# Kernel optimization log

Hardware: AMD Instinct MI355X
Metric: run time of the kernel (lower is better)

## Reference

```python
import jax, jax.numpy as jnp
import numpy as np

D_MODEL = 1024
NUM_HEADS = 16
D_HEAD = D_MODEL // NUM_HEADS


def _rope(x):
    """Rotary embedding, lucidrains interleaved convention, applied along axis -2.

    x: (..., n, d). Positions are arange(n); freq_i = 10000**(-2i/d), each freq
    repeated twice (interleaved); rotate_half swaps adjacent pairs (-x2, x1).
    """
    n, d = x.shape[-2], x.shape[-1]
    inv_freq = 1.0 / (10000.0 ** (jnp.arange(0, d, 2, dtype=jnp.float32) / d))  # (d/2,)
    freqs = jnp.arange(n, dtype=jnp.float32)[:, None] * inv_freq[None, :]       # (n, d/2)
    emb = jnp.repeat(freqs, 2, axis=-1)                                         # (n, d)
    cos, sin = jnp.cos(emb).astype(x.dtype), jnp.sin(emb).astype(x.dtype)
    xp = x.reshape(x.shape[:-1] + (d // 2, 2))
    rot = jnp.stack([-xp[..., 1], xp[..., 0]], axis=-1).reshape(x.shape)
    return x * cos + rot * sin


def setup_inputs() -> dict:
    key = jax.random.key(0)
    ks = jax.random.split(key, 11)
    B, S = 4, 2048
    mk = lambda k, shape: (jax.random.normal(k, shape, dtype=jnp.float32) * 0.02)
    return {
        "query": jax.random.normal(ks[0], (B, S, D_MODEL), dtype=jnp.float32),
        "key": jax.random.normal(ks[1], (B, S, D_MODEL), dtype=jnp.float32),
        "value": jax.random.normal(ks[2], (B, S, D_MODEL), dtype=jnp.float32),
        "Wq": mk(ks[3], (D_MODEL, D_MODEL)), "bq": jnp.zeros((D_MODEL,), jnp.float32),
        "Wk": mk(ks[4], (D_MODEL, D_MODEL)), "bk": jnp.zeros((D_MODEL,), jnp.float32),
        "Wv": mk(ks[5], (D_MODEL, D_MODEL)), "bv": jnp.zeros((D_MODEL,), jnp.float32),
        "Wo": mk(ks[6], (D_MODEL, D_MODEL)), "bo": jnp.zeros((D_MODEL,), jnp.float32),
    }


def reference(query, key, value, Wq, bq, Wk, bk, Wv, bv, Wo, bo):
    B, S, _ = query.shape
    H, dh = NUM_HEADS, D_HEAD
    # projections (torch Linear: x @ W.T + b)
    q = (query @ Wq.T + bq).reshape(B, S, H, dh)           # (b, t, h, d)
    k = (key @ Wk.T + bk).reshape(B, S, H, dh).transpose(0, 2, 1, 3)   # (b, h, t, d)
    v = (value @ Wv.T + bv).reshape(B, S, H, dh).transpose(0, 2, 1, 3)  # (b, h, t, d)
    # Faithful to source: query rotated along axis -2 = HEADS axis (pre-permute),
    # key rotated along axis -2 = time axis.
    q = _rope(q)                                            # positions over heads (source quirk)
    k = _rope(k)                                            # positions over time
    q = q.transpose(0, 2, 1, 3)                             # (b, h, t, d)
    scores = jnp.einsum("bhqd,bhkd->bhqk", q, k) / jnp.sqrt(jnp.float32(D_MODEL))
    attn = jax.nn.softmax(scores, axis=-1)
    ctx = jnp.einsum("bhqk,bhkd->bhqd", attn, v)            # (b, h, t, d)
    ctx = ctx.transpose(0, 2, 1, 3).reshape(B, S, H * dh)   # (b, t, d_model)
    return ctx @ Wo.T + bo
```

## Files before the change

### kernel.cpp

```cpp
#include <hip/hip_runtime.h>

using u16 = unsigned short;
typedef __bf16 bf16x8 __attribute__((ext_vector_type(8)));
typedef __bf16 bf16x2 __attribute__((ext_vector_type(2)));
typedef float f32x4 __attribute__((ext_vector_type(4)));

#if __has_builtin(__builtin_amdgcn_exp2f)
#define QSCALE 0.04508422468443852f
#define FEXP(x) __builtin_amdgcn_exp2f(x)
#else
#define QSCALE 0.03125f
#define FEXP(x) __expf(x)
#endif

__device__ __forceinline__ u16 f2bf(float f) {
  unsigned u = __builtin_bit_cast(unsigned, f);
  u += 0x7FFFu + ((u >> 16) & 1u);
  return (u16)(u >> 16);
}

#define GLD_LDS16(g, l)                                                                   \
  __builtin_amdgcn_global_load_lds((const __attribute__((address_space(1))) void*)(g),    \
                                   (__attribute__((address_space(3))) void*)(l), 16, 0, 0)

template <int LOG2NB>
__global__ void cvt_multi(const float* __restrict__ i0, const float* __restrict__ i1,
                          const float* __restrict__ i2, const float* __restrict__ i3,
                          u16* __restrict__ o0, u16* __restrict__ o1, u16* __restrict__ o2,
                          u16* __restrict__ o3, int n4) {
  const int which = blockIdx.x >> LOG2NB;
  const float* in = which == 0 ? i0 : which == 1 ? i1 : which == 2 ? i2 : i3;
  u16* out = which == 0 ? o0 : which == 1 ? o1 : which == 2 ? o2 : o3;
  int i = (blockIdx.x & ((1 << LOG2NB) - 1)) * blockDim.x + threadIdx.x;
  const int st = (1 << LOG2NB) * blockDim.x;
  for (; i < n4; i += st) {
    float4 v = reinterpret_cast<const float4*>(in)[i];
    ushort4 o = make_ushort4(f2bf(v.x), f2bf(v.y), f2bf(v.z), f2bf(v.w));
    reinterpret_cast<ushort4*>(out)[i] = o;
  }
}

template <int EPI>
__global__ __launch_bounds__(512, 4) void gemm_bt(const u16* __restrict__ A,
                                                  const u16* __restrict__ Bt,
                                                  const float* __restrict__ bias,
                                                  void* __restrict__ outp) {
  __shared__ u16 lA[3][128 * 32];
  __shared__ u16 lB[3][128 * 32];
  const int tid = threadIdx.x;
  const int l = tid & 63, w = tid >> 6;
  const int wr = w >> 2, wc = w & 3;
  const int l15 = l & 15, lg = l >> 4;
  const int rsw = (l15 >> 1) & 3;
  const int bid = ((blockIdx.x & 7) << 6) | (blockIdx.x >> 3);
  const int br = bid >> 3, bc = bid & 7;

  f32x4 acc[4][2];
#pragma unroll
  for (int m = 0; m < 4; ++m)
#pragma unroll
    for (int n = 0; n < 2; ++n) acc[m][n] = f32x4{0.f, 0.f, 0.f, 0.f};

  const int srow = tid >> 2;
  const int gch = (tid & 3) ^ ((tid >> 3) & 3);
  const u16* Abase = A + (size_t)(br * 128 + srow) * 1024 + gch * 8;
  const u16* Bbase = Bt + (size_t)(bc * 128 + srow) * 1024 + gch * 8;

  auto stage = [&](int buf, int kk) {
    GLD_LDS16(Abase + kk, &lA[buf][tid * 8]);
    GLD_LDS16(Bbase + kk, &lB[buf][tid * 8]);
  };

  auto compute = [&](int cur) {
    const int c = ((lg ^ rsw) << 3);
    bf16x8 af[4], bfr[2];
#pragma unroll
    for (int m = 0; m < 4; ++m)
      af[m] = *reinterpret_cast<const bf16x8*>(&lA[cur][(wr * 64 + m * 16 + l15) * 32 + c]);
#pragma unroll
    for (int n = 0; n < 2; ++n)
      bfr[n] = *reinterpret_cast<const bf16x8*>(&lB[cur][(wc * 32 + n * 16 + l15) * 32 + c]);
#pragma unroll
    for (int m = 0; m < 4; ++m)
#pragma unroll
      for (int n = 0; n < 2; ++n)
        acc[m][n] = __builtin_amdgcn_mfma_f32_16x16x32_bf16(af[m], bfr[n], acc[m][n], 0, 0, 0);
  };

  stage(0, 0);
  stage(1, 32);
  asm volatile("s_waitcnt vmcnt(2)" ::: "memory");
  __builtin_amdgcn_s_barrier();
  __builtin_amdgcn_sched_barrier(0);

  int cur = 0, nx2 = 2;
  for (int it = 0; it < 31; ++it) {
    if (it < 30) stage(nx2, (it + 2) * 32);
    compute(cur);
    if (it < 30)
      asm volatile("s_waitcnt vmcnt(2)" ::: "memory");
    else
      asm volatile("s_waitcnt vmcnt(0)" ::: "memory");
    __builtin_amdgcn_s_barrier();
    __builtin_amdgcn_sched_barrier(0);
    cur = cur == 2 ? 0 : cur + 1;
    nx2 = nx2 == 2 ? 0 : nx2 + 1;
  }
  compute(cur);

  const int row0 = br * 128 + wr * 64;
  const int col0 = bc * 128 + wc * 32;

  if constexpr (EPI == 0 || EPI == 1) {
    u16* out = reinterpret_cast<u16*>(outp);
#pragma unroll
    for (int n = 0; n < 2; ++n) {
      const int gn = col0 + n * 16 + l15;
      const float bv2 = bias[gn];
      const int p = (gn & 63) >> 1;
      const float invf = __expf((float)p * -0.28782313663f);
      float ss = 0.f, cc = 0.f;
      if constexpr (EPI == 0) {
        const float th = (float)(gn >> 6) * invf;
        sincosf(th, &ss, &cc);
      }
#pragma unroll
      for (int m = 0; m < 4; ++m) {
        const int gm0 = row0 + m * 16 + lg * 4;
#pragma unroll
        for (int r = 0; r < 4; ++r) {
          float x = acc[m][n][r] + bv2;
          if constexpr (EPI == 1) {
            const float th = (float)((gm0 + r) & 2047) * invf;
            sincosf(th, &ss, &cc);
          }
          const float xp = __shfl_xor(x, 1);
          float o = (gn & 1) ? fmaf(xp, ss, x * cc) : fmaf(-xp, ss, x * cc);
          if constexpr (EPI == 0) o *= QSCALE;
          out[(size_t)(gm0 + r) * 1024 + gn] = f2bf(o);
        }
      }
    }
  } else if constexpr (EPI == 2) {
    u16* vT = reinterpret_cast<u16*>(outp);
#pragma unroll
    for (int n = 0; n < 2; ++n) {
      const int gn = col0 + n * 16 + l15;
      const float bv2 = bias[gn];
      const int hh = gn >> 6, dd = gn & 63;
#pragma unroll
      for (int m = 0; m < 4; ++m) {
        const int gm0 = row0 + m * 16 + lg * 4;
        const int bb = gm0 >> 11, s0 = gm0 & 2047;
        ushort4 pk = make_ushort4(f2bf(acc[m][n][0] + bv2), f2bf(acc[m][n][1] + bv2),
                                  f2bf(acc[m][n][2] + bv2), f2bf(acc[m][n][3] + bv2));
        *reinterpret_cast<ushort4*>(vT + ((size_t)((bb * 16 + hh) * 64 + dd) * 2048 + s0)) = pk;
      }
    }
  } else {
    float* out = reinterpret_cast<float*>(outp);
#pragma unroll
    for (int n = 0; n < 2; ++n) {
      const int gn = col0 + n * 16 + l15;
      const float bv2 = bias[gn];
#pragma unroll
      for (int m = 0; m < 4; ++m) {
        const int gm0 = row0 + m * 16 + lg * 4;
#pragma unroll
        for (int r = 0; r < 4; ++r) out[(size_t)(gm0 + r) * 1024 + gn] = acc[m][n][r] + bv2;
      }
    }
  }
}

__global__ __launch_bounds__(512, 6) void attn_fwd(const u16* __restrict__ Q,
                                                   const u16* __restrict__ K,
                                                   const u16* __restrict__ Vt,
                                                   u16* __restrict__ ctx) {
  __shared__ u16 sK[3][64 * 64];
  __shared__ u16 sV[3][64 * 64];
  const int tid = threadIdx.x;
  const int l = tid & 63, w = tid >> 6;
  const int l15 = l & 15, lg = l >> 4;
  const int swz = (l15 & 7) << 3;
  const int wgid = ((blockIdx.x & 7) << 7) | (blockIdx.x >> 3);
  const int qt = wgid & 15, bh = wgid >> 4;
  const int b = bh >> 4, h = bh & 15;

  bf16x8 qf0, qf1;
  {
    const u16* qp = Q + (size_t)(b * 2048 + qt * 128 + w * 16 + l15) * 1024 + h * 64 + lg * 8;
    qf0 = *reinterpret_cast<const bf16x8*>(qp);
    qf1 = *reinterpret_cast<const bf16x8*>(qp + 32);
  }

  bf16x8 ones;
#pragma unroll
  for (int i = 0; i < 8; ++i) ones[i] = (__bf16)1.0f;

  f32x4 acc_l = f32x4{0.f, 0.f, 0.f, 0.f};
  f32x4 acc_o[4];
#pragma unroll
  for (int n = 0; n < 4; ++n) acc_o[n] = f32x4{0.f, 0.f, 0.f, 0.f};

  const int srow = tid >> 3;
  const int scol = ((tid & 7) ^ (srow & 7)) * 8;
  const int krow = (srow & 0x23) | ((srow & 0x0C) << 1) | ((srow & 0x10) >> 2);
  const u16* Kbase = K + (size_t)(b * 2048 + krow) * 1024 + h * 64 + scol;
  const u16* Vbase = Vt + (size_t)(bh * 64 + srow) * 2048 + scol;

  auto stage = [&](int buf, int j) {
    GLD_LDS16(Kbase + (size_t)(j * 64) * 1024, &sK[buf][tid * 8]);
    GLD_LDS16(Vbase + j * 64, &sV[buf][tid * 8]);
  };

  stage(0, 0);
  stage(1, 1);
  asm volatile("s_waitcnt vmcnt(2)" ::: "memory");
  __builtin_amdgcn_s_barrier();
  __builtin_amdgcn_sched_barrier(0);

  int cur = 0, nx2 = 2;
  for (int j = 0; j < 32; ++j) {
    if (j < 30) stage(nx2, j + 2);

    f32x4 accs[4];
#pragma unroll
    for (int nk = 0; nk < 4; ++nk) accs[nk] = f32x4{0.f, 0.f, 0.f, 0.f};
    const int c0 = (lg * 8) ^ swz;
    __builtin_amdgcn_s_setprio(1);
#pragma unroll
    for (int nk = 0; nk < 4; ++nk) {
      bf16x8 kf0 = *reinterpret_cast<const bf16x8*>(&sK[cur][(nk * 16 + l15) * 64 + c0]);
      bf16x8 kf1 = *reinterpret_cast<const bf16x8*>(&sK[cur][(nk * 16 + l15) * 64 + (c0 ^ 32)]);
      accs[nk] = __builtin_amdgcn_mfma_f32_16x16x32_bf16(kf0, qf0, accs[nk], 0, 0, 0);
      accs[nk] = __builtin_amdgcn_mfma_f32_16x16x32_bf16(kf1, qf1, accs[nk], 0, 0, 0);
    }
    __builtin_amdgcn_s_setprio(0);

    unsigned wpk[4][2];
#pragma unroll
    for (int nk = 0; nk < 4; ++nk) {
      const float p0 = FEXP(accs[nk][0]), p1 = FEXP(accs[nk][1]);
      const float p2 = FEXP(accs[nk][2]), p3 = FEXP(accs[nk][3]);
      bf16x2 t0, t1;
      t0.x = (__bf16)p0; t0.y = (__bf16)p1;
      t1.x = (__bf16)p2; t1.y = (__bf16)p3;
      wpk[nk][0] = __builtin_bit_cast(unsigned, t0);
      wpk[nk][1] = __builtin_bit_cast(unsigned, t1);
    }

    __builtin_amdgcn_s_setprio(1);
#pragma unroll
    for (int ks = 0; ks < 2; ++ks) {
      const uint4 paw = make_uint4(wpk[2 * ks][0], wpk[2 * ks][1],
                                   wpk[2 * ks + 1][0], wpk[2 * ks + 1][1]);
      const bf16x8 pa = __builtin_bit_cast(bf16x8, paw);
      acc_l = __builtin_amdgcn_mfma_f32_16x16x32_bf16(ones, pa, acc_l, 0, 0, 0);
#pragma unroll
      for (int n = 0; n < 4; ++n) {
        bf16x8 vf = *reinterpret_cast<const bf16x8*>(
            &sV[cur][(n * 16 + l15) * 64 + ((ks * 32 + lg * 8) ^ swz)]);
        acc_o[n] = __builtin_amdgcn_mfma_f32_16x16x32_bf16(vf, pa, acc_o[n], 0, 0, 0);
      }
    }
    __builtin_amdgcn_s_setprio(0);

    if (j < 31) {
      if (j < 30)
        asm volatile("s_waitcnt vmcnt(2)" ::: "memory");
      else
        asm volatile("s_waitcnt vmcnt(0)" ::: "memory");
      __builtin_amdgcn_s_barrier();
      __builtin_amdgcn_sched_barrier(0);
    }
    cur = cur == 2 ? 0 : cur + 1;
    nx2 = nx2 == 2 ? 0 : nx2 + 1;
  }

  const float inv = 1.f / acc_l[0];
  u16* obase = ctx + (size_t)(b * 2048 + qt * 128 + w * 16 + l15) * 1024 + h * 64;
#pragma unroll
  for (int n = 0; n < 4; ++n) {
    ushort4 pk = make_ushort4(f2bf(acc_o[n][0] * inv), f2bf(acc_o[n][1] * inv),
                              f2bf(acc_o[n][2] * inv), f2bf(acc_o[n][3] * inv));
    *reinterpret_cast<ushort4*>(obase + n * 16 + lg * 4) = pk;
  }
}

extern "C" void kernel_launch(void* const* d_in, const int* in_sizes, int n_in, void* d_out,
                              int out_size, void* d_ws, size_t ws_size, hipStream_t stream) {
  (void)in_sizes; (void)n_in; (void)out_size; (void)ws_size;
  const float* query = (const float*)d_in[0];
  const float* key = (const float*)d_in[1];
  const float* value = (const float*)d_in[2];
  const float* Wq = (const float*)d_in[3];
  const float* bq = (const float*)d_in[4];
  const float* Wk = (const float*)d_in[5];
  const float* bk = (const float*)d_in[6];
  const float* Wv = (const float*)d_in[7];
  const float* bv = (const float*)d_in[8];
  const float* Wo = (const float*)d_in[9];
  const float* bo = (const float*)d_in[10];

  char* ws = (char*)d_ws;
  const size_t MB = (size_t)1 << 20;
  u16* xq = (u16*)(ws + 0 * MB);
  u16* xk = (u16*)(ws + 16 * MB);
  u16* xv = (u16*)(ws + 32 * MB);
  u16* wqb = (u16*)(ws + 48 * MB);
  u16* wkb = (u16*)(ws + 50 * MB);
  u16* wvb = (u16*)(ws + 52 * MB);
  u16* wob = (u16*)(ws + 54 * MB);
  u16* qb = (u16*)(ws + 56 * MB);
  u16* kb = (u16*)(ws + 72 * MB);
  u16* vT = (u16*)(ws + 88 * MB);
  u16* cx = (u16*)(ws + 104 * MB);

  cvt_multi<9><<<1536, 256, 0, stream>>>(query, key, value, query, xq, xk, xv, xq, 2097152);
  cvt_multi<6><<<256, 256, 0, stream>>>(Wq, Wk, Wv, Wo, wqb, wkb, wvb, wob, 262144);

  gemm_bt<0><<<512, 512, 0, stream>>>(xq, wqb, bq, qb);
  gemm_bt<1><<<512, 512, 0, stream>>>(xk, wkb, bk, kb);
  gemm_bt<2><<<512, 512, 0, stream>>>(xv, wvb, bv, vT);
  attn_fwd<<<1024, 512, 0, stream>>>(qb, kb, vT, cx);
  gemm_bt<3><<<512, 512, 0, stream>>>(cx, wob, bo, (float*)d_out);
}
```

Baseline: 218.3 us.

## Merge convert kernels, widen GEMM K-tile, double attention block size

Merges the two fp32-to-bf16 conversion launches into one kernel. Changes the GEMM pipeline from a 3-stage K=32 ring to a 2-stage K=64 double buffer, so there are half as many barriers per K step. Doubles the attention workgroup to 1024 threads covering 256 query rows, with half the threads loading K and half loading V, so each K/V tile is reused by twice as many queries. The costs are less prefetch depth in the GEMM (it now waits vmcnt(0) every iteration) and higher register and occupancy pressure in attention.

```diff
diff --git a/kernel.cpp b/kernel.cpp
--- a/kernel.cpp
+++ b/kernel.cpp
@@ -23,19 +23,32 @@
   __builtin_amdgcn_global_load_lds((const __attribute__((address_space(1))) void*)(g),    \
                                    (__attribute__((address_space(3))) void*)(l), 16, 0, 0)
 
-template <int LOG2NB>
-__global__ void cvt_multi(const float* __restrict__ i0, const float* __restrict__ i1,
-                          const float* __restrict__ i2, const float* __restrict__ i3,
-                          u16* __restrict__ o0, u16* __restrict__ o1, u16* __restrict__ o2,
-                          u16* __restrict__ o3, int n4) {
-  const int which = blockIdx.x >> LOG2NB;
-  const float* in = which == 0 ? i0 : which == 1 ? i1 : which == 2 ? i2 : i3;
-  u16* out = which == 0 ? o0 : which == 1 ? o1 : which == 2 ? o2 : o3;
-  int i = (blockIdx.x & ((1 << LOG2NB) - 1)) * blockDim.x + threadIdx.x;
-  const int st = (1 << LOG2NB) * blockDim.x;
+__global__ void cvt_all(const float* __restrict__ q, const float* __restrict__ k,
+                        const float* __restrict__ v, const float* __restrict__ wq,
+                        const float* __restrict__ wk, const float* __restrict__ wv,
+                        const float* __restrict__ wo, u16* __restrict__ oq,
+                        u16* __restrict__ ok, u16* __restrict__ ov, u16* __restrict__ owq,
+                        u16* __restrict__ owk, u16* __restrict__ owv, u16* __restrict__ owo) {
+  const float* in;
+  u16* out;
+  int n4, base, nb;
+  const int bidx = blockIdx.x;
+  if (bidx < 1536) {
+    const int which = bidx >> 9;
+    in = which == 0 ? q : which == 1 ? k : v;
+    out = which == 0 ? oq : which == 1 ? ok : ov;
+    n4 = 2097152; base = bidx & 511; nb = 512;
+  } else {
+    const int which = (bidx - 1536) >> 6;
+    in = which == 0 ? wq : which == 1 ? wk : which == 2 ? wv : wo;
+    out = which == 0 ? owq : which == 1 ? owk : which == 2 ? owv : owo;
+    n4 = 262144; base = (bidx - 1536) & 63; nb = 64;
+  }
+  int i = base * blockDim.x + threadIdx.x;
+  const int st = nb * blockDim.x;
   for (; i < n4; i += st) {
-    float4 v = reinterpret_cast<const float4*>(in)[i];
-    ushort4 o = make_ushort4(f2bf(v.x), f2bf(v.y), f2bf(v.z), f2bf(v.w));
+    float4 x = reinterpret_cast<const float4*>(in)[i];
+    ushort4 o = make_ushort4(f2bf(x.x), f2bf(x.y), f2bf(x.z), f2bf(x.w));
     reinterpret_cast<ushort4*>(out)[i] = o;
   }
 }
@@ -45,13 +58,12 @@
                                                   const u16* __restrict__ Bt,
                                                   const float* __restrict__ bias,
                                                   void* __restrict__ outp) {
-  __shared__ u16 lA[3][128 * 32];
-  __shared__ u16 lB[3][128 * 32];
+  __shared__ u16 lA[2][128 * 64];
+  __shared__ u16 lB[2][128 * 64];
   const int tid = threadIdx.x;
   const int l = tid & 63, w = tid >> 6;
   const int wr = w >> 2, wc = w & 3;
   const int l15 = l & 15, lg = l >> 4;
-  const int rsw = (l15 >> 1) & 3;
   const int bid = ((blockIdx.x & 7) << 6) | (blockIdx.x >> 3);
   const int br = bid >> 3, bc = bid & 7;
 
@@ -61,52 +73,52 @@
 #pragma unroll
     for (int n = 0; n < 2; ++n) acc[m][n] = f32x4{0.f, 0.f, 0.f, 0.f};
 
-  const int srow = tid >> 2;
-  const int gch = (tid & 3) ^ ((tid >> 3) & 3);
+  const int srow = tid >> 3;
+  const int gch = (tid & 7) ^ (srow & 7);
   const u16* Abase = A + (size_t)(br * 128 + srow) * 1024 + gch * 8;
   const u16* Bbase = Bt + (size_t)(bc * 128 + srow) * 1024 + gch * 8;
 
   auto stage = [&](int buf, int kk) {
     GLD_LDS16(Abase + kk, &lA[buf][tid * 8]);
+    GLD_LDS16(Abase + (size_t)64 * 1024 + kk, &lA[buf][4096 + tid * 8]);
     GLD_LDS16(Bbase + kk, &lB[buf][tid * 8]);
+    GLD_LDS16(Bbase + (size_t)64 * 1024 + kk, &lB[buf][4096 + tid * 8]);
   };
 
   auto compute = [&](int cur) {
-    const int c = ((lg ^ rsw) << 3);
-    bf16x8 af[4], bfr[2];
-#pragma unroll
-    for (int m = 0; m < 4; ++m)
-      af[m] = *reinterpret_cast<const bf16x8*>(&lA[cur][(wr * 64 + m * 16 + l15) * 32 + c]);
-#pragma unroll
-    for (int n = 0; n < 2; ++n)
-      bfr[n] = *reinterpret_cast<const bf16x8*>(&lB[cur][(wc * 32 + n * 16 + l15) * 32 + c]);
-#pragma unroll
-    for (int m = 0; m < 4; ++m)
+#pragma unroll
+    for (int ks = 0; ks < 2; ++ks) {
+      const int c = (((ks * 4 + lg) ^ (l15 & 7)) << 3);
+      bf16x8 af[4], bfr[2];
+#pragma unroll
+      for (int m = 0; m < 4; ++m)
+        af[m] = *reinterpret_cast<const bf16x8*>(&lA[cur][(wr * 64 + m * 16 + l15) * 64 + c]);
 #pragma unroll
       for (int n = 0; n < 2; ++n)
-        acc[m][n] = __builtin_amdgcn_mfma_f32_16x16x32_bf16(af[m], bfr[n], acc[m][n], 0, 0, 0);
+        bfr[n] = *reinterpret_cast<const bf16x8*>(&lB[cur][(wc * 32 + n * 16 + l15) * 64 + c]);
+#pragma unroll
+      for (int m = 0; m < 4; ++m)
+#pragma unroll
+        for (int n = 0; n < 2; ++n)
+          acc[m][n] = __builtin_amdgcn_mfma_f32_16x16x32_bf16(af[m], bfr[n], acc[m][n], 0, 0, 0);
+    }
   };
 
   stage(0, 0);
-  stage(1, 32);
-  asm volatile("s_waitcnt vmcnt(2)" ::: "memory");
+  asm volatile("s_waitcnt vmcnt(0)" ::: "memory");
   __builtin_amdgcn_s_barrier();
   __builtin_amdgcn_sched_barrier(0);
 
-  int cur = 0, nx2 = 2;
-  for (int it = 0; it < 31; ++it) {
-    if (it < 30) stage(nx2, (it + 2) * 32);
+  for (int it = 0; it < 16; ++it) {
+    const int cur = it & 1;
+    if (it < 15) stage(cur ^ 1, (it + 1) * 64);
     compute(cur);
-    if (it < 30)
-      asm volatile("s_waitcnt vmcnt(2)" ::: "memory");
-    else
+    if (it < 15) {
       asm volatile("s_waitcnt vmcnt(0)" ::: "memory");
-    __builtin_amdgcn_s_barrier();
-    __builtin_amdgcn_sched_barrier(0);
-    cur = cur == 2 ? 0 : cur + 1;
-    nx2 = nx2 == 2 ? 0 : nx2 + 1;
-  }
-  compute(cur);
+      __builtin_amdgcn_s_barrier();
+      __builtin_amdgcn_sched_barrier(0);
+    }
+  }
 
   const int row0 = br * 128 + wr * 64;
   const int col0 = bc * 128 + wc * 32;
@@ -173,23 +185,24 @@
   }
 }
 
-__global__ __launch_bounds__(512, 6) void attn_fwd(const u16* __restrict__ Q,
-                                                   const u16* __restrict__ K,
-                                                   const u16* __restrict__ Vt,
-                                                   u16* __restrict__ ctx) {
+__global__ __launch_bounds__(1024, 8) void attn_fwd(const u16* __restrict__ Q,
+                                                    const u16* __restrict__ K,
+                                                    const u16* __restrict__ Vt,
+                                                    u16* __restrict__ ctx) {
   __shared__ u16 sK[3][64 * 64];
   __shared__ u16 sV[3][64 * 64];
   const int tid = threadIdx.x;
   const int l = tid & 63, w = tid >> 6;
   const int l15 = l & 15, lg = l >> 4;
   const int swz = (l15 & 7) << 3;
-  const int wgid = ((blockIdx.x & 7) << 7) | (blockIdx.x >> 3);
-  const int qt = wgid & 15, bh = wgid >> 4;
+  const int wgid = ((blockIdx.x & 7) << 6) | (blockIdx.x >> 3);
+  const int qt = wgid & 7, bh = wgid >> 3;
   const int b = bh >> 4, h = bh & 15;
 
   bf16x8 qf0, qf1;
   {
-    const u16* qp = Q + (size_t)(b * 2048 + qt * 128 + w * 16 + l15) * 1024 + h * 64 + lg * 8;
+    const u16* qp =
+        Q + (size_t)(b * 2048 + qt * 256 + w * 16 + l15) * 1024 + h * 64 + lg * 8;
     qf0 = *reinterpret_cast<const bf16x8*>(qp);
     qf1 = *reinterpret_cast<const bf16x8*>(qp + 32);
   }
@@ -203,20 +216,24 @@
 #pragma unroll
   for (int n = 0; n < 4; ++n) acc_o[n] = f32x4{0.f, 0.f, 0.f, 0.f};
 
-  const int srow = tid >> 3;
-  const int scol = ((tid & 7) ^ (srow & 7)) * 8;
+  const int stid = tid & 511;
+  const int srow = stid >> 3;
+  const int scol = ((stid & 7) ^ (srow & 7)) * 8;
   const int krow = (srow & 0x23) | ((srow & 0x0C) << 1) | ((srow & 0x10) >> 2);
   const u16* Kbase = K + (size_t)(b * 2048 + krow) * 1024 + h * 64 + scol;
   const u16* Vbase = Vt + (size_t)(bh * 64 + srow) * 2048 + scol;
+  const bool isK = tid < 512;
 
   auto stage = [&](int buf, int j) {
-    GLD_LDS16(Kbase + (size_t)(j * 64) * 1024, &sK[buf][tid * 8]);
-    GLD_LDS16(Vbase + j * 64, &sV[buf][tid * 8]);
+    if (isK)
+      GLD_LDS16(Kbase + (size_t)(j * 64) * 1024, &sK[buf][stid * 8]);
+    else
+      GLD_LDS16(Vbase + j * 64, &sV[buf][stid * 8]);
   };
 
   stage(0, 0);
   stage(1, 1);
-  asm volatile("s_waitcnt vmcnt(2)" ::: "memory");
+  asm volatile("s_waitcnt vmcnt(1)" ::: "memory");
   __builtin_amdgcn_s_barrier();
   __builtin_amdgcn_sched_barrier(0);
 
@@ -224,10 +241,11 @@
   for (int j = 0; j < 32; ++j) {
     if (j < 30) stage(nx2, j + 2);
 
+    const int c0 = (lg * 8) ^ swz;
     f32x4 accs[4];
 #pragma unroll
     for (int nk = 0; nk < 4; ++nk) accs[nk] = f32x4{0.f, 0.f, 0.f, 0.f};
-    const int c0 = (lg * 8) ^ swz;
+
     __builtin_amdgcn_s_setprio(1);
 #pragma unroll
     for (int nk = 0; nk < 4; ++nk) {
@@ -268,7 +286,7 @@
 
     if (j < 31) {
       if (j < 30)
-        asm volatile("s_waitcnt vmcnt(2)" ::: "memory");
+        asm volatile("s_waitcnt vmcnt(1)" ::: "memory");
       else
         asm volatile("s_waitcnt vmcnt(0)" ::: "memory");
       __builtin_amdgcn_s_barrier();
@@ -279,7 +297,7 @@
   }
 
   const float inv = 1.f / acc_l[0];
-  u16* obase = ctx + (size_t)(b * 2048 + qt * 128 + w * 16 + l15) * 1024 + h * 64;
+  u16* obase = ctx + (size_t)(b * 2048 + qt * 256 + w * 16 + l15) * 1024 + h * 64;
 #pragma unroll
   for (int n = 0; n < 4; ++n) {
     ushort4 pk = make_ushort4(f2bf(acc_o[n][0] * inv), f2bf(acc_o[n][1] * inv),
@@ -317,12 +335,12 @@
   u16* vT = (u16*)(ws + 88 * MB);
   u16* cx = (u16*)(ws + 104 * MB);
 
-  cvt_multi<9><<<1536, 256, 0, stream>>>(query, key, value, query, xq, xk, xv, xq, 2097152);
-  cvt_multi<6><<<256, 256, 0, stream>>>(Wq, Wk, Wv, Wo, wqb, wkb, wvb, wob, 262144);
+  cvt_all<<<1792, 256, 0, stream>>>(query, key, value, Wq, Wk, Wv, Wo, xq, xk, xv, wqb, wkb,
+                                    wvb, wob);
 
   gemm_bt<0><<<512, 512, 0, stream>>>(xq, wqb, bq, qb);
   gemm_bt<1><<<512, 512, 0, stream>>>(xk, wkb, bk, kb);
   gemm_bt<2><<<512, 512, 0, stream>>>(xv, wvb, bv, vT);
-  attn_fwd<<<1024, 512, 0, stream>>>(qb, kb, vT, cx);
+  attn_fwd<<<512, 1024, 0, stream>>>(qb, kb, vT, cx);
   gemm_bt<3><<<512, 512, 0, stream>>>(cx, wob, bo, (float*)d_out);
 }
```

Result: faster. 200.7 us (-8.1%).
